# Optimization experiments

Measured on AMD Instinct MI355X. Metric: run time of the kernel, lower is better.

Reference implementation:

```python
import jax, jax.numpy as jnp
import numpy as np

NR = 4      # num_real
NC = 6      # num_complex_conjugate_pairs
L = 2       # num_layers (hidden->hidden blocks)
H = 64      # hidden_dim
B, S = 32, 2048
C = NR + 2 * NC


def setup_inputs() -> dict:
    key = jax.random.key(0)
    ks = jax.random.split(key, 9)
    s = 0.1
    return {
        "z": jax.random.normal(ks[0], (B, S, C), jnp.float32),
        "W0_r": jax.random.normal(ks[1], (NR, H), jnp.float32) * s,
        "b0_r": jnp.zeros((NR, H), jnp.float32),
        "Wm_r": jax.random.normal(ks[2], (L, NR, H, H), jnp.float32) * s,
        "bm_r": jnp.zeros((L, NR, H), jnp.float32),
        "Wl_r": jax.random.normal(ks[3], (NR, H, 1), jnp.float32) * s,
        "bl_r": jnp.zeros((NR, 1), jnp.float32),
        "W0_c": jax.random.normal(ks[4], (NC, H), jnp.float32) * s,
        "b0_c": jnp.zeros((NC, H), jnp.float32),
        "Wm_c": jax.random.normal(ks[5], (L, NC, H, H), jnp.float32) * s,
        "bm_c": jnp.zeros((L, NC, H), jnp.float32),
        "Wl_c": jax.random.normal(ks[6], (NC, H, 2), jnp.float32) * s,
        "bl_c": jnp.zeros((NC, 2), jnp.float32),
    }


def _channel_mlps(x, W0, b0, Wm, bm, Wl, bl):
    # x: [F, P] scalar input per channel; runs P independent tiny MLPs.
    h = jax.nn.relu(x[:, :, None] * W0[None] + b0[None])  # [F, P, H]
    for l in range(Wm.shape[0]):  # small fixed layer count
        h = jax.nn.relu(jnp.einsum('fph,phk->fpk', h, Wm[l]) + bm[l][None])
    return jnp.einsum('fph,pho->fpo', h, Wl) + bl[None]  # [F, P, out]


def reference(z, W0_r, b0_r, Wm_r, bm_r, Wl_r, bl_r,
              W0_c, b0_c, Wm_c, bm_c, Wl_c, bl_c):
    b_, s_, c_ = z.shape
    zf = z.reshape(-1, c_)                       # [F, C]
    # real channels
    zr = zf[:, :NR]                              # [F, NR]
    real_lambda = _channel_mlps(zr, W0_r, b0_r, Wm_r, bm_r, Wl_r, bl_r)[..., 0]
    # complex-conjugate pairs
    zc = zf[:, NR:].reshape(-1, NC, 2)           # [F, NC, 2]
    z1, z2 = zc[..., 0], zc[..., 1]
    z_mag = z1 * z1 + z2 * z2                    # [F, NC]
    mo = _channel_mlps(z_mag, W0_c, b0_c, Wm_c, bm_c, Wl_c, bl_c)  # [F, NC, 2]
    mu, omega = mo[..., 0], mo[..., 1]
    mu_exp = jnp.exp(mu)
    mc = mu_exp * jnp.cos(omega)
    ms = mu_exp * jnp.sin(omega)
    # z_pred = z @ K with K block-diagonal: diag(real_lambda) then 2x2 rotations
    out_r = zr * real_lambda                     # [F, NR]
    # row-vector times 2x2 block [[mc, -ms], [ms, mc]]
    o1 = z1 * mc + z2 * ms
    o2 = -z1 * ms + z2 * mc
    out_c = jnp.stack([o1, o2], axis=-1).reshape(-1, 2 * NC)
    return jnp.concatenate([out_r, out_c], axis=-1).reshape(b_, s_, c_)
```

## Files before the change

### kernel.cpp

```cpp
#include <hip/hip_runtime.h>
#include <cstdint>

#define NRC 4
#define NCC 6
#define HD 64
#define CW 16

typedef _Float16 half8 __attribute__((ext_vector_type(8)));
typedef float f32x4 __attribute__((ext_vector_type(4)));

__device__ __forceinline__ uint32_t pkh(float a, float b) {
    auto h = __builtin_amdgcn_cvt_pkrtz(a, b);
    return __builtin_bit_cast(uint32_t, h);
}

__global__ __launch_bounds__(256, 3) void koop_kernel(
    const float* __restrict__ z,
    const float* __restrict__ W0_r, const float* __restrict__ b0_r,
    const float* __restrict__ Wm_r, const float* __restrict__ bm_r,
    const float* __restrict__ Wl_r, const float* __restrict__ bl_r,
    const float* __restrict__ W0_c, const float* __restrict__ b0_c,
    const float* __restrict__ Wm_c, const float* __restrict__ bm_c,
    const float* __restrict__ Wl_c, const float* __restrict__ bl_c,
    float* __restrict__ out)
{
    __shared__ uint32_t smem[12800];

    const int tid  = threadIdx.x;
    const int lane = tid & 63;
    const int wv   = tid >> 6;
    const int bid  = blockIdx.x;
    const int ch   = bid >> 8;
    const int tile = bid & 255;
    const int t0   = tile * 256;

    const bool isReal = (ch < NRC);
    const int  pc     = ch - NRC;
    const int  No     = isReal ? 1 : 2;

    const float* W0 = isReal ? (W0_r + ch * HD) : (W0_c + pc * HD);
    const float* b0 = isReal ? (b0_r + ch * HD) : (b0_c + pc * HD);
    const float* Wl = isReal ? (Wl_r + ch * HD) : (Wl_c + pc * HD * 2);
    const float* bl = isReal ? (bl_r + ch)      : (bl_c + pc * 2);

    {
        const int nH = tid & 63;
        const int bb = (tid >> 6) * 2;
        for (int l = 0; l < 2; ++l) {
            const float* Wm = isReal ? (Wm_r + (l * NRC + ch) * HD * HD)
                                     : (Wm_c + (l * NCC + pc) * HD * HD);
            #pragma unroll
            for (int r = 0; r < 2; ++r) {
                const int blk = bb + r;
                const float* src = Wm + blk * 8 * HD + nH;
                float v0 = src[0],       v1 = src[HD],     v2 = src[2*HD], v3 = src[3*HD];
                float v4 = src[4*HD],    v5 = src[5*HD],   v6 = src[6*HD], v7 = src[7*HD];
                const int woff = l * 2048 + nH * 32 + (((blk + nH) & 7) << 2);
                uint4 q = { pkh(v0, v1), pkh(v2, v3), pkh(v4, v5), pkh(v6, v7) };
                *(uint4*)&smem[woff] = q;
            }
        }
    }
    __syncthreads();

    const int t = t0 + wv * 64 + lane;
    float xin = 0.f, z1 = 0.f, z2 = 0.f, sval;
    if (isReal) {
        xin = z[t * CW + ch];
        sval = xin;
    } else {
        float2 zz = *(const float2*)(z + t * CW + NRC + 2 * pc);
        z1 = zz.x; z2 = zz.y;
        sval = z1 * z1 + z2 * z2;
    }

    const int hbase = 4096 + wv * 2048;
    {
        #pragma unroll
        for (int blk = 0; blk < 8; ++blk) {
            uint32_t q0, q1, q2, q3;
            {
                const int n = blk * 8;
                float a0 = fmaxf(fmaf(sval, W0[n+0], b0[n+0]), 0.f);
                float a1 = fmaxf(fmaf(sval, W0[n+1], b0[n+1]), 0.f);
                float a2 = fmaxf(fmaf(sval, W0[n+2], b0[n+2]), 0.f);
                float a3 = fmaxf(fmaf(sval, W0[n+3], b0[n+3]), 0.f);
                float a4 = fmaxf(fmaf(sval, W0[n+4], b0[n+4]), 0.f);
                float a5 = fmaxf(fmaf(sval, W0[n+5], b0[n+5]), 0.f);
                float a6 = fmaxf(fmaf(sval, W0[n+6], b0[n+6]), 0.f);
                float a7 = fmaxf(fmaf(sval, W0[n+7], b0[n+7]), 0.f);
                q0 = pkh(a0, a1); q1 = pkh(a2, a3); q2 = pkh(a4, a5); q3 = pkh(a6, a7);
            }
            const int woff = hbase + lane * 32 + (((blk + lane) & 7) << 2);
            uint4 q = { q0, q1, q2, q3 };
            *(uint4*)&smem[woff] = q;
        }
    }

    const int l15 = lane & 15;
    const int g   = lane >> 4;

    f32x4 acc[4][4];
    for (int l = 0; l < 2; ++l) {
        half8 A[4][2];
        #pragma unroll
        for (int m = 0; m < 4; ++m) {
            #pragma unroll
            for (int kt = 0; kt < 2; ++kt) {
                const int row = m * 16 + l15;
                const int blk = kt * 4 + g;
                A[m][kt] = *(const half8*)&smem[l * 2048 + row * 32 + (((blk + row) & 7) << 2)];
            }
        }
        const float* bm = isReal ? (bm_r + (l * NRC + ch) * HD)
                                 : (bm_c + (l * NCC + pc) * HD);
        f32x4 bv[4];
        #pragma unroll
        for (int m = 0; m < 4; ++m)
            bv[m] = *(const f32x4*)(bm + m * 16 + g * 4);

        #pragma unroll
        for (int m = 0; m < 4; ++m)
            #pragma unroll
            for (int tt = 0; tt < 4; ++tt)
                acc[m][tt] = (f32x4){0.f, 0.f, 0.f, 0.f};

        #pragma unroll
        for (int tt = 0; tt < 4; ++tt) {
            #pragma unroll
            for (int kt = 0; kt < 2; ++kt) {
                const int row = tt * 16 + l15;
                const int blk = kt * 4 + g;
                half8 Bf = *(const half8*)&smem[hbase + row * 32 + (((blk + row) & 7) << 2)];
                #pragma unroll
                for (int m = 0; m < 4; ++m)
                    acc[m][tt] = __builtin_amdgcn_mfma_f32_16x16x32_f16(A[m][kt], Bf, acc[m][tt], 0, 0, 0);
            }
        }

        #pragma unroll
        for (int tt = 0; tt < 4; ++tt) {
            const int row = tt * 16 + l15;
            #pragma unroll
            for (int m = 0; m < 4; ++m) {
                f32x4 v = acc[m][tt];
                float a0 = fmaxf(v[0] + bv[m][0], 0.f);
                float a1 = fmaxf(v[1] + bv[m][1], 0.f);
                float a2 = fmaxf(v[2] + bv[m][2], 0.f);
                float a3 = fmaxf(v[3] + bv[m][3], 0.f);
                const int blk  = 2 * m + (g >> 1);
                const int woff = hbase + row * 32 + (((blk + row) & 7) << 2) + (g & 1) * 2;
                uint2 q = { pkh(a0, a1), pkh(a2, a3) };
                *(uint2*)&smem[woff] = q;
            }
        }
    }

    half8 Af[2];
    #pragma unroll
    for (int kt = 0; kt < 2; ++kt) {
        half8 a;
        #pragma unroll
        for (int e = 0; e < 8; ++e) {
            const int k = kt * 32 + g * 8 + e;
            float w = (l15 < No) ? Wl[k * No + l15] : 0.f;
            a[e] = (_Float16)w;
        }
        Af[kt] = a;
    }
    f32x4 accf[4];
    #pragma unroll
    for (int tt = 0; tt < 4; ++tt) accf[tt] = (f32x4){0.f, 0.f, 0.f, 0.f};
    #pragma unroll
    for (int tt = 0; tt < 4; ++tt) {
        #pragma unroll
        for (int kt = 0; kt < 2; ++kt) {
            const int row = tt * 16 + l15;
            const int blk = kt * 4 + g;
            half8 Bf = *(const half8*)&smem[hbase + row * 32 + (((blk + row) & 7) << 2)];
            accf[tt] = __builtin_amdgcn_mfma_f32_16x16x32_f16(Af[kt], Bf, accf[tt], 0, 0, 0);
        }
    }

    float* smf = (float*)smem;
    const int obase = 12288 + wv * 128;
    if (g == 0) {
        #pragma unroll
        for (int tt = 0; tt < 4; ++tt) {
            const int tok = tt * 16 + l15;
            if (isReal) {
                smf[obase + tok * 2] = accf[tt][0] + bl[0];
            } else {
                float2 mo = { accf[tt][0] + bl[0], accf[tt][1] + bl[1] };
                *(float2*)&smf[obase + tok * 2] = mo;
            }
        }
    }
    __syncthreads();

    if (isReal) {
        float lam = smf[obase + lane * 2];
        out[t * CW + ch] = xin * lam;
    } else {
        float2 mo = *(const float2*)&smf[obase + lane * 2];
        float ex = __expf(mo.x);
        float mc = ex * __cosf(mo.y);
        float ms = ex * __sinf(mo.y);
        float o1 =  z1 * mc + z2 * ms;
        float o2 =  z2 * mc - z1 * ms;
        *(float2*)(out + t * CW + NRC + 2 * pc) = make_float2(o1, o2);
    }
}

extern "C" void kernel_launch(void* const* d_in, const int* in_sizes, int n_in,
                              void* d_out, int out_size, void* d_ws, size_t ws_size,
                              hipStream_t stream) {
    (void)in_sizes; (void)n_in; (void)d_ws; (void)ws_size; (void)out_size;
    const float* z    = (const float*)d_in[0];
    const float* W0_r = (const float*)d_in[1];
    const float* b0_r = (const float*)d_in[2];
    const float* Wm_r = (const float*)d_in[3];
    const float* bm_r = (const float*)d_in[4];
    const float* Wl_r = (const float*)d_in[5];
    const float* bl_r = (const float*)d_in[6];
    const float* W0_c = (const float*)d_in[7];
    const float* b0_c = (const float*)d_in[8];
    const float* Wm_c = (const float*)d_in[9];
    const float* bm_c = (const float*)d_in[10];
    const float* Wl_c = (const float*)d_in[11];
    const float* bl_c = (const float*)d_in[12];
    float* outp = (float*)d_out;

    dim3 grid(2560), block(256);
    koop_kernel<<<grid, block, 0, stream>>>(z, W0_r, b0_r, Wm_r, bm_r, Wl_r, bl_r,
                                            W0_c, b0_c, Wm_c, bm_c, Wl_c, bl_c, outp);
}
```

Before: 29.65 us.

## Shrink LDS footprint, preload layer-0 weights to registers, raise occupancy

Layer-0 weight fragments are now loaded into registers before the activation buffers are written, so the activation area can reuse that LDS space and the shared array shrinks. The launch bound goes from 3 to 4 blocks per CU. Hidden-layer biases and output biases are folded into the MFMA accumulator initialisation. The layer loop is split into two token halves to reduce live accumulators. The final block-wide barrier becomes a per-wave LDS waitcnt, since each wave only reads its own output slots. The risks are register pressure from the extra preloaded fragments, and relying on intra-wave LDS ordering for correctness.

```diff
diff --git a/kernel.cpp b/kernel.cpp
--- a/kernel.cpp
+++ b/kernel.cpp
@@ -14,7 +14,7 @@
     return __builtin_bit_cast(uint32_t, h);
 }
 
-__global__ __launch_bounds__(256, 3) void koop_kernel(
+__global__ __launch_bounds__(256, 4) void koop_kernel(
     const float* __restrict__ z,
     const float* __restrict__ W0_r, const float* __restrict__ b0_r,
     const float* __restrict__ Wm_r, const float* __restrict__ bm_r,
@@ -24,7 +24,7 @@
     const float* __restrict__ Wl_c, const float* __restrict__ bl_c,
     float* __restrict__ out)
 {
-    __shared__ uint32_t smem[12800];
+    __shared__ uint32_t smem[10240];
 
     const int tid  = threadIdx.x;
     const int lane = tid & 63;
@@ -49,16 +49,32 @@
         for (int l = 0; l < 2; ++l) {
             const float* Wm = isReal ? (Wm_r + (l * NRC + ch) * HD * HD)
                                      : (Wm_c + (l * NCC + pc) * HD * HD);
+            const int base = l ? 8192 : 0;
             #pragma unroll
             for (int r = 0; r < 2; ++r) {
                 const int blk = bb + r;
                 const float* src = Wm + blk * 8 * HD + nH;
                 float v0 = src[0],       v1 = src[HD],     v2 = src[2*HD], v3 = src[3*HD];
                 float v4 = src[4*HD],    v5 = src[5*HD],   v6 = src[6*HD], v7 = src[7*HD];
-                const int woff = l * 2048 + nH * 32 + (((blk + nH) & 7) << 2);
+                const int woff = base + nH * 32 + (((blk + nH) & 7) << 2);
                 uint4 q = { pkh(v0, v1), pkh(v2, v3), pkh(v4, v5), pkh(v6, v7) };
                 *(uint4*)&smem[woff] = q;
             }
+        }
+    }
+    __syncthreads();
+
+    const int l15 = lane & 15;
+    const int g   = lane >> 4;
+
+    half8 A1[4][2];
+    #pragma unroll
+    for (int m = 0; m < 4; ++m) {
+        #pragma unroll
+        for (int kt = 0; kt < 2; ++kt) {
+            const int row = m * 16 + l15;
+            const int blk = kt * 4 + g;
+            A1[m][kt] = *(const half8*)&smem[row * 32 + (((blk + row) & 7) << 2)];
         }
     }
     __syncthreads();
@@ -74,7 +90,7 @@
         sval = z1 * z1 + z2 * z2;
     }
 
-    const int hbase = 4096 + wv * 2048;
+    const int hbase = wv * 2048;
     {
         #pragma unroll
         for (int blk = 0; blk < 8; ++blk) {
@@ -97,19 +113,23 @@
         }
     }
 
-    const int l15 = lane & 15;
-    const int g   = lane >> 4;
-
-    f32x4 acc[4][4];
+    half8 A[4][2];
+    #pragma unroll
+    for (int m = 0; m < 4; ++m)
+        #pragma unroll
+        for (int kt = 0; kt < 2; ++kt)
+            A[m][kt] = A1[m][kt];
+
     for (int l = 0; l < 2; ++l) {
-        half8 A[4][2];
-        #pragma unroll
-        for (int m = 0; m < 4; ++m) {
-            #pragma unroll
-            for (int kt = 0; kt < 2; ++kt) {
-                const int row = m * 16 + l15;
-                const int blk = kt * 4 + g;
-                A[m][kt] = *(const half8*)&smem[l * 2048 + row * 32 + (((blk + row) & 7) << 2)];
+        if (l == 1) {
+            #pragma unroll
+            for (int m = 0; m < 4; ++m) {
+                #pragma unroll
+                for (int kt = 0; kt < 2; ++kt) {
+                    const int row = m * 16 + l15;
+                    const int blk = kt * 4 + g;
+                    A[m][kt] = *(const half8*)&smem[8192 + row * 32 + (((blk + row) & 7) << 2)];
+                }
             }
         }
         const float* bm = isReal ? (bm_r + (l * NRC + ch) * HD)
@@ -120,38 +140,44 @@
             bv[m] = *(const f32x4*)(bm + m * 16 + g * 4);
 
         #pragma unroll
-        for (int m = 0; m < 4; ++m)
-            #pragma unroll
-            for (int tt = 0; tt < 4; ++tt)
-                acc[m][tt] = (f32x4){0.f, 0.f, 0.f, 0.f};
-
-        #pragma unroll
-        for (int tt = 0; tt < 4; ++tt) {
-            #pragma unroll
-            for (int kt = 0; kt < 2; ++kt) {
+        for (int th = 0; th < 2; ++th) {
+            f32x4 acc[4][2];
+            #pragma unroll
+            for (int m = 0; m < 4; ++m)
+                #pragma unroll
+                for (int u = 0; u < 2; ++u)
+                    acc[m][u] = bv[m];
+
+            #pragma unroll
+            for (int u = 0; u < 2; ++u) {
+                const int tt = th * 2 + u;
+                #pragma unroll
+                for (int kt = 0; kt < 2; ++kt) {
+                    const int row = tt * 16 + l15;
+                    const int blk = kt * 4 + g;
+                    half8 Bf = *(const half8*)&smem[hbase + row * 32 + (((blk + row) & 7) << 2)];
+                    #pragma unroll
+                    for (int m = 0; m < 4; ++m)
+                        acc[m][u] = __builtin_amdgcn_mfma_f32_16x16x32_f16(A[m][kt], Bf, acc[m][u], 0, 0, 0);
+                }
+            }
+
+            #pragma unroll
+            for (int u = 0; u < 2; ++u) {
+                const int tt = th * 2 + u;
                 const int row = tt * 16 + l15;
-                const int blk = kt * 4 + g;
-                half8 Bf = *(const half8*)&smem[hbase + row * 32 + (((blk + row) & 7) << 2)];
-                #pragma unroll
-                for (int m = 0; m < 4; ++m)
-                    acc[m][tt] = __builtin_amdgcn_mfma_f32_16x16x32_f16(A[m][kt], Bf, acc[m][tt], 0, 0, 0);
-            }
-        }
-
-        #pragma unroll
-        for (int tt = 0; tt < 4; ++tt) {
-            const int row = tt * 16 + l15;
-            #pragma unroll
-            for (int m = 0; m < 4; ++m) {
-                f32x4 v = acc[m][tt];
-                float a0 = fmaxf(v[0] + bv[m][0], 0.f);
-                float a1 = fmaxf(v[1] + bv[m][1], 0.f);
-                float a2 = fmaxf(v[2] + bv[m][2], 0.f);
-                float a3 = fmaxf(v[3] + bv[m][3], 0.f);
-                const int blk  = 2 * m + (g >> 1);
-                const int woff = hbase + row * 32 + (((blk + row) & 7) << 2) + (g & 1) * 2;
-                uint2 q = { pkh(a0, a1), pkh(a2, a3) };
-                *(uint2*)&smem[woff] = q;
+                #pragma unroll
+                for (int m = 0; m < 4; ++m) {
+                    f32x4 v = acc[m][u];
+                    float a0 = fmaxf(v[0], 0.f);
+                    float a1 = fmaxf(v[1], 0.f);
+                    float a2 = fmaxf(v[2], 0.f);
+                    float a3 = fmaxf(v[3], 0.f);
+                    const int blk  = 2 * m + (g >> 1);
+                    const int woff = hbase + row * 32 + (((blk + row) & 7) << 2) + (g & 1) * 2;
+                    uint2 q = { pkh(a0, a1), pkh(a2, a3) };
+                    *(uint2*)&smem[woff] = q;
+                }
             }
         }
     }
@@ -168,9 +194,11 @@
         }
         Af[kt] = a;
     }
+    f32x4 cf0 = (f32x4){0.f, 0.f, 0.f, 0.f};
+    if (g == 0) { cf0[0] = bl[0]; if (!isReal) cf0[1] = bl[1]; }
     f32x4 accf[4];
     #pragma unroll
-    for (int tt = 0; tt < 4; ++tt) accf[tt] = (f32x4){0.f, 0.f, 0.f, 0.f};
+    for (int tt = 0; tt < 4; ++tt) accf[tt] = cf0;
     #pragma unroll
     for (int tt = 0; tt < 4; ++tt) {
         #pragma unroll
@@ -183,20 +211,21 @@
     }
 
     float* smf = (float*)smem;
-    const int obase = 12288 + wv * 128;
+    const int obase = hbase;
     if (g == 0) {
         #pragma unroll
         for (int tt = 0; tt < 4; ++tt) {
             const int tok = tt * 16 + l15;
             if (isReal) {
-                smf[obase + tok * 2] = accf[tt][0] + bl[0];
+                smf[obase + tok * 2] = accf[tt][0];
             } else {
-                float2 mo = { accf[tt][0] + bl[0], accf[tt][1] + bl[1] };
+                float2 mo = { accf[tt][0], accf[tt][1] };
                 *(float2*)&smf[obase + tok * 2] = mo;
             }
         }
     }
-    __syncthreads();
+    __asm__ volatile("s_waitcnt lgkmcnt(0)" ::: "memory");
+    __builtin_amdgcn_sched_barrier(0);
 
     if (isReal) {
         float lam = smf[obase + lane * 2];
```

Measured after the change: 26.79 us. 9.6% less time.

## Split each block's tokens across eight waves with 32 tokens per wave

Applied to the files above, without the earlier changes.

Doubles the block to 512 threads so each wave processes 32 tokens instead of 64, halving per-wave accumulators and shared activation space. It spreads the weight staging across more threads, folds the biases into the MFMA accumulator initialisation, and replaces the final block barrier with a wave-local LDS wait. This is meant to raise occupancy and latency hiding. The cost is that half the lanes idle in the epilogue, and barrier cost rises with the larger block.

```diff
diff --git a/kernel.cpp b/kernel.cpp
--- a/kernel.cpp
+++ b/kernel.cpp
@@ -14,7 +14,7 @@
     return __builtin_bit_cast(uint32_t, h);
 }
 
-__global__ __launch_bounds__(256, 3) void koop_kernel(
+__global__ __launch_bounds__(512, 6) void koop_kernel(
     const float* __restrict__ z,
     const float* __restrict__ W0_r, const float* __restrict__ b0_r,
     const float* __restrict__ Wm_r, const float* __restrict__ bm_r,
@@ -24,7 +24,7 @@
     const float* __restrict__ Wl_c, const float* __restrict__ bl_c,
     float* __restrict__ out)
 {
-    __shared__ uint32_t smem[12800];
+    __shared__ uint32_t smem[12288];
 
     const int tid  = threadIdx.x;
     const int lane = tid & 63;
@@ -43,27 +43,12 @@
     const float* Wl = isReal ? (Wl_r + ch * HD) : (Wl_c + pc * HD * 2);
     const float* bl = isReal ? (bl_r + ch)      : (bl_c + pc * 2);
 
-    {
-        const int nH = tid & 63;
-        const int bb = (tid >> 6) * 2;
-        for (int l = 0; l < 2; ++l) {
-            const float* Wm = isReal ? (Wm_r + (l * NRC + ch) * HD * HD)
-                                     : (Wm_c + (l * NCC + pc) * HD * HD);
-            #pragma unroll
-            for (int r = 0; r < 2; ++r) {
-                const int blk = bb + r;
-                const float* src = Wm + blk * 8 * HD + nH;
-                float v0 = src[0],       v1 = src[HD],     v2 = src[2*HD], v3 = src[3*HD];
-                float v4 = src[4*HD],    v5 = src[5*HD],   v6 = src[6*HD], v7 = src[7*HD];
-                const int woff = l * 2048 + nH * 32 + (((blk + nH) & 7) << 2);
-                uint4 q = { pkh(v0, v1), pkh(v2, v3), pkh(v4, v5), pkh(v6, v7) };
-                *(uint4*)&smem[woff] = q;
-            }
-        }
-    }
-    __syncthreads();
-
-    const int t = t0 + wv * 64 + lane;
+    const int l15  = lane & 15;
+    const int g    = lane >> 4;
+    const int tokl = lane & 31;
+    const int hf   = lane >> 5;
+
+    const int t = t0 + wv * 32 + tokl;
     float xin = 0.f, z1 = 0.f, z2 = 0.f, sval;
     if (isReal) {
         xin = z[t * CW + ch];
@@ -74,141 +59,147 @@
         sval = z1 * z1 + z2 * z2;
     }
 
-    const int hbase = 4096 + wv * 2048;
+    half8 Af[2];
+    #pragma unroll
+    for (int kt = 0; kt < 2; ++kt) {
+        half8 a;
+        #pragma unroll
+        for (int e = 0; e < 8; ++e) {
+            const int k = kt * 32 + g * 8 + e;
+            float w = (l15 < No) ? Wl[k * No + l15] : 0.f;
+            a[e] = (_Float16)w;
+        }
+        Af[kt] = a;
+    }
+
     {
-        #pragma unroll
-        for (int blk = 0; blk < 8; ++blk) {
-            uint32_t q0, q1, q2, q3;
-            {
-                const int n = blk * 8;
-                float a0 = fmaxf(fmaf(sval, W0[n+0], b0[n+0]), 0.f);
-                float a1 = fmaxf(fmaf(sval, W0[n+1], b0[n+1]), 0.f);
-                float a2 = fmaxf(fmaf(sval, W0[n+2], b0[n+2]), 0.f);
-                float a3 = fmaxf(fmaf(sval, W0[n+3], b0[n+3]), 0.f);
-                float a4 = fmaxf(fmaf(sval, W0[n+4], b0[n+4]), 0.f);
-                float a5 = fmaxf(fmaf(sval, W0[n+5], b0[n+5]), 0.f);
-                float a6 = fmaxf(fmaf(sval, W0[n+6], b0[n+6]), 0.f);
-                float a7 = fmaxf(fmaf(sval, W0[n+7], b0[n+7]), 0.f);
-                q0 = pkh(a0, a1); q1 = pkh(a2, a3); q2 = pkh(a4, a5); q3 = pkh(a6, a7);
-            }
-            const int woff = hbase + lane * 32 + (((blk + lane) & 7) << 2);
-            uint4 q = { q0, q1, q2, q3 };
+        const int nH  = tid & 63;
+        const int blk = tid >> 6;
+        #pragma unroll
+        for (int l = 0; l < 2; ++l) {
+            const float* Wm = isReal ? (Wm_r + (l * NRC + ch) * HD * HD)
+                                     : (Wm_c + (l * NCC + pc) * HD * HD);
+            const float* src = Wm + blk * 8 * HD + nH;
+            float v0 = src[0],    v1 = src[HD],   v2 = src[2*HD], v3 = src[3*HD];
+            float v4 = src[4*HD], v5 = src[5*HD], v6 = src[6*HD], v7 = src[7*HD];
+            const int woff = l * 2048 + nH * 32 + (((blk + nH) & 7) << 2);
+            uint4 q = { pkh(v0, v1), pkh(v2, v3), pkh(v4, v5), pkh(v6, v7) };
             *(uint4*)&smem[woff] = q;
         }
     }
-
-    const int l15 = lane & 15;
-    const int g   = lane >> 4;
-
-    f32x4 acc[4][4];
+    __syncthreads();
+
+    const int hb = 4096 + wv * 1024;
+    #pragma unroll
+    for (int j = 0; j < 4; ++j) {
+        const int blk = hf * 4 + j;
+        const int n = blk * 8;
+        float a0 = fmaxf(fmaf(sval, W0[n+0], b0[n+0]), 0.f);
+        float a1 = fmaxf(fmaf(sval, W0[n+1], b0[n+1]), 0.f);
+        float a2 = fmaxf(fmaf(sval, W0[n+2], b0[n+2]), 0.f);
+        float a3 = fmaxf(fmaf(sval, W0[n+3], b0[n+3]), 0.f);
+        float a4 = fmaxf(fmaf(sval, W0[n+4], b0[n+4]), 0.f);
+        float a5 = fmaxf(fmaf(sval, W0[n+5], b0[n+5]), 0.f);
+        float a6 = fmaxf(fmaf(sval, W0[n+6], b0[n+6]), 0.f);
+        float a7 = fmaxf(fmaf(sval, W0[n+7], b0[n+7]), 0.f);
+        const int woff = hb + tokl * 32 + (((blk + tokl) & 7) << 2);
+        uint4 q = { pkh(a0, a1), pkh(a2, a3), pkh(a4, a5), pkh(a6, a7) };
+        *(uint4*)&smem[woff] = q;
+    }
+
     for (int l = 0; l < 2; ++l) {
-        half8 A[4][2];
+        const float* bm = isReal ? (bm_r + (l * NRC + ch) * HD)
+                                 : (bm_c + (l * NCC + pc) * HD);
+        f32x4 acc[4][2];
         #pragma unroll
         for (int m = 0; m < 4; ++m) {
+            f32x4 bv = *(const f32x4*)(bm + m * 16 + g * 4);
+            acc[m][0] = bv;
+            acc[m][1] = bv;
+        }
+
+        #pragma unroll
+        for (int kt = 0; kt < 2; ++kt) {
+            half8 A[4];
             #pragma unroll
-            for (int kt = 0; kt < 2; ++kt) {
+            for (int m = 0; m < 4; ++m) {
                 const int row = m * 16 + l15;
                 const int blk = kt * 4 + g;
-                A[m][kt] = *(const half8*)&smem[l * 2048 + row * 32 + (((blk + row) & 7) << 2)];
-            }
-        }
-        const float* bm = isReal ? (bm_r + (l * NRC + ch) * HD)
-                                 : (bm_c + (l * NCC + pc) * HD);
-        f32x4 bv[4];
-        #pragma unroll
-        for (int m = 0; m < 4; ++m)
-            bv[m] = *(const f32x4*)(bm + m * 16 + g * 4);
-
-        #pragma unroll
-        for (int m = 0; m < 4; ++m)
+                A[m] = *(const half8*)&smem[l * 2048 + row * 32 + (((blk + row) & 7) << 2)];
+            }
             #pragma unroll
-            for (int tt = 0; tt < 4; ++tt)
-                acc[m][tt] = (f32x4){0.f, 0.f, 0.f, 0.f};
-
-        #pragma unroll
-        for (int tt = 0; tt < 4; ++tt) {
-            #pragma unroll
-            for (int kt = 0; kt < 2; ++kt) {
+            for (int tt = 0; tt < 2; ++tt) {
                 const int row = tt * 16 + l15;
                 const int blk = kt * 4 + g;
-                half8 Bf = *(const half8*)&smem[hbase + row * 32 + (((blk + row) & 7) << 2)];
+                half8 Bf = *(const half8*)&smem[hb + row * 32 + (((blk + row) & 7) << 2)];
                 #pragma unroll
                 for (int m = 0; m < 4; ++m)
-                    acc[m][tt] = __builtin_amdgcn_mfma_f32_16x16x32_f16(A[m][kt], Bf, acc[m][tt], 0, 0, 0);
-            }
-        }
-
-        #pragma unroll
-        for (int tt = 0; tt < 4; ++tt) {
+                    acc[m][tt] = __builtin_amdgcn_mfma_f32_16x16x32_f16(A[m], Bf, acc[m][tt], 0, 0, 0);
+            }
+        }
+
+        #pragma unroll
+        for (int tt = 0; tt < 2; ++tt) {
             const int row = tt * 16 + l15;
             #pragma unroll
             for (int m = 0; m < 4; ++m) {
                 f32x4 v = acc[m][tt];
-                float a0 = fmaxf(v[0] + bv[m][0], 0.f);
-                float a1 = fmaxf(v[1] + bv[m][1], 0.f);
-                float a2 = fmaxf(v[2] + bv[m][2], 0.f);
-                float a3 = fmaxf(v[3] + bv[m][3], 0.f);
+                float a0 = fmaxf(v[0], 0.f);
+                float a1 = fmaxf(v[1], 0.f);
+                float a2 = fmaxf(v[2], 0.f);
+                float a3 = fmaxf(v[3], 0.f);
                 const int blk  = 2 * m + (g >> 1);
-                const int woff = hbase + row * 32 + (((blk + row) & 7) << 2) + (g & 1) * 2;
+                const int woff = hb + row * 32 + (((blk + row) & 7) << 2) + (g & 1) * 2;
                 uint2 q = { pkh(a0, a1), pkh(a2, a3) };
                 *(uint2*)&smem[woff] = q;
             }
         }
     }
 
-    half8 Af[2];
+    f32x4 cf0 = (f32x4){0.f, 0.f, 0.f, 0.f};
+    if (g == 0) { cf0[0] = bl[0]; if (!isReal) cf0[1] = bl[1]; }
+    f32x4 accf[2] = { cf0, cf0 };
     #pragma unroll
     for (int kt = 0; kt < 2; ++kt) {
-        half8 a;
-        #pragma unroll
-        for (int e = 0; e < 8; ++e) {
-            const int k = kt * 32 + g * 8 + e;
-            float w = (l15 < No) ? Wl[k * No + l15] : 0.f;
-            a[e] = (_Float16)w;
-        }
-        Af[kt] = a;
-    }
-    f32x4 accf[4];
-    #pragma unroll
-    for (int tt = 0; tt < 4; ++tt) accf[tt] = (f32x4){0.f, 0.f, 0.f, 0.f};
-    #pragma unroll
-    for (int tt = 0; tt < 4; ++tt) {
-        #pragma unroll
-        for (int kt = 0; kt < 2; ++kt) {
+        #pragma unroll
+        for (int tt = 0; tt < 2; ++tt) {
             const int row = tt * 16 + l15;
             const int blk = kt * 4 + g;
-            half8 Bf = *(const half8*)&smem[hbase + row * 32 + (((blk + row) & 7) << 2)];
+            half8 Bf = *(const half8*)&smem[hb + row * 32 + (((blk + row) & 7) << 2)];
             accf[tt] = __builtin_amdgcn_mfma_f32_16x16x32_f16(Af[kt], Bf, accf[tt], 0, 0, 0);
         }
     }
 
     float* smf = (float*)smem;
-    const int obase = 12288 + wv * 128;
+    const int obase = hb;
     if (g == 0) {
         #pragma unroll
-        for (int tt = 0; tt < 4; ++tt) {
+        for (int tt = 0; tt < 2; ++tt) {
             const int tok = tt * 16 + l15;
             if (isReal) {
-                smf[obase + tok * 2] = accf[tt][0] + bl[0];
+                smf[obase + tok * 2] = accf[tt][0];
             } else {
-                float2 mo = { accf[tt][0] + bl[0], accf[tt][1] + bl[1] };
+                float2 mo = { accf[tt][0], accf[tt][1] };
                 *(float2*)&smf[obase + tok * 2] = mo;
             }
         }
     }
-    __syncthreads();
-
-    if (isReal) {
-        float lam = smf[obase + lane * 2];
-        out[t * CW + ch] = xin * lam;
-    } else {
-        float2 mo = *(const float2*)&smf[obase + lane * 2];
-        float ex = __expf(mo.x);
-        float mc = ex * __cosf(mo.y);
-        float ms = ex * __sinf(mo.y);
-        float o1 =  z1 * mc + z2 * ms;
-        float o2 =  z2 * mc - z1 * ms;
-        *(float2*)(out + t * CW + NRC + 2 * pc) = make_float2(o1, o2);
+    __asm__ volatile("s_waitcnt lgkmcnt(0)" ::: "memory");
+    __builtin_amdgcn_sched_barrier(0);
+
+    if (hf == 0) {
+        if (isReal) {
+            float lam = smf[obase + tokl * 2];
+            out[t * CW + ch] = xin * lam;
+        } else {
+            float2 mo = *(const float2*)&smf[obase + tokl * 2];
+            float ex = __expf(mo.x);
+            float mc = ex * __cosf(mo.y);
+            float ms = ex * __sinf(mo.y);
+            float o1 =  z1 * mc + z2 * ms;
+            float o2 =  z2 * mc - z1 * ms;
+            *(float2*)(out + t * CW + NRC + 2 * pc) = make_float2(o1, o2);
+        }
     }
 }
 
@@ -231,7 +222,7 @@
     const float* bl_c = (const float*)d_in[12];
     float* outp = (float*)d_out;
 
-    dim3 grid(2560), block(256);
+    dim3 grid(2560), block(512);
     koop_kernel<<<grid, block, 0, stream>>>(z, W0_r, b0_r, Wm_r, bm_r, Wl_r, bl_r,
                                             W0_c, b0_c, Wm_c, bm_c, Wl_c, bl_c, outp);
 }
```

Measured after the change: 44.76 us. 1.51x slower.
